# Optimization experiments

Hardware: AMD Instinct MI355X
Metric: run time of the kernel (lower is better)

Reference implementation:

```python
import jax, jax.numpy as jnp
import numpy as np

# --- Instant-NGP hash-grid constants (from __init__ defaults) ---
T = 2 ** 19          # hash table size per level
NLEVELS = 16
F = 2                # features per level
L = 4                # dir positional-encoding frequencies
LEVELS = np.geomspace(16, 2048, NLEVELS, dtype=int)            # grid resolutions
PRIMES = jnp.array([1, 2654435761, 805459861], dtype=jnp.uint32)
FREQS = (2.0 ** np.arange(L)).astype(np.float32)
# corner c in 0..7 -> bit b_i = use ceil along dim i (matches torch corner order)
BITS = jnp.array([[(c >> i) & 1 for i in range(3)] for c in range(8)], dtype=bool)  # (8,3)


def _hash_encode(pos, table):
    """pos: (P,3) level-scaled positions; table: (T,F). Returns (P,F).
    Spatial hash + gather + trilinear interpolation (== grid_sample trick)."""
    fl = jnp.floor(pos)
    ce = jnp.ceil(pos)
    frac = pos - fl                                             # (P,3) in [0,1)
    corners = jnp.where(BITS[None], ce[:, None, :], fl[:, None, :]).astype(jnp.int32)  # (P,8,3)
    # uint32 wrap-around arithmetic matches torch int64 mod 2^19 (T is a power of 2)
    v = corners.astype(jnp.uint32) * PRIMES                     # (P,8,3)
    h = (v[..., 0] ^ v[..., 1] ^ v[..., 2]) & jnp.uint32(T - 1) # (P,8)
    cf = table[h]                                               # (P,8,F) irregular gather
    w = jnp.prod(jnp.where(BITS[None], frac[:, None, :], 1.0 - frac[:, None, :]), axis=-1)  # (P,8)
    return jnp.einsum('pc,pcf->pf', w, cf)


def setup_inputs() -> dict:
    key = jax.random.key(0)
    ks = jax.random.split(key, 16)
    N, S = 2048, 192
    # positions s.t. x*scene_scale + 0.5 lies mostly in (0,1), a few outside (mask path)
    x = (jax.random.uniform(ks[0], (N, S, 3), jnp.float32) - 0.5) * 1.1
    r_dir = jax.random.normal(ks[1], (N, S, 3), jnp.float32)
    tables = jax.random.normal(ks[2], (NLEVELS, T, F), jnp.float32) * 1e-4

    def lin(k, fan_in, fan_out):
        return jax.random.normal(k, (fan_in, fan_out), jnp.float32) / np.float32(np.sqrt(fan_in))

    din = F * NLEVELS              # 32
    cin = 16 + 3 + 3 * L * 2       # 43
    return {
        'x': x, 'r_dir': r_dir, 'tables': tables,
        'dW1': lin(ks[3], din, 64), 'db1': jnp.zeros((64,), jnp.float32),
        'dW2': lin(ks[4], 64, 16), 'db2': jnp.zeros((16,), jnp.float32),
        'cW1': lin(ks[5], cin, 64), 'cb1': jnp.zeros((64,), jnp.float32),
        'cW2': lin(ks[6], 64, 64), 'cb2': jnp.zeros((64,), jnp.float32),
        'cW3': lin(ks[7], 64, 3), 'cb3': jnp.zeros((3,), jnp.float32),
    }


def reference(x, r_dir, tables, dW1, db1, dW2, db2, cW1, cb1, cW2, cb2, cW3, cb3):
    scene_scale = 1.0
    N, S = x.shape[0], r_dir.shape[1]
    xf = x.reshape(-1, 3) * scene_scale + 0.5          # (P,3)
    rd = r_dir.reshape(-1, 3)                          # (P,3)
    mask = jnp.all(xf > 0, axis=-1) & jnp.all(xf < 1, axis=-1)  # (P,)

    # multi-resolution hash encoding (fixed 16-level loop, vectorized over points)
    feats = jnp.concatenate(
        [_hash_encode(xf * np.float32(LEVELS[i]), tables[i]) for i in range(NLEVELS)],
        axis=-1)                                       # (P, F*NLEVELS)

    log_sigma = jax.nn.relu(feats @ dW1 + db1) @ dW2 + db2        # (P,16)

    # direction positional encoding: [dir, sin(2^l*2pi*dir), cos(...)] -> (P, 3+3*2L)
    xin = rd[..., None] * (2.0 * np.pi * jnp.asarray(FREQS))      # (P,3,L)
    enc = jnp.concatenate([jnp.sin(xin), jnp.cos(xin)], axis=-1).reshape(rd.shape[0], -1)
    enc_dir = jnp.concatenate([rd, enc], axis=-1)                 # (P,27)

    h = jax.nn.relu(jnp.concatenate([log_sigma, enc_dir], axis=-1) @ cW1 + cb1)
    h = jax.nn.relu(h @ cW2 + cb2)
    color = jax.nn.sigmoid(h @ cW3 + cb3)                         # (P,3)

    color = jnp.where(mask[:, None], color, 0.0)
    sigma = jnp.where(mask[:, None], jnp.exp(log_sigma[:, :1]), 0.0)
    return color.reshape(N, S, 3), sigma.reshape(N, S, 1)
```

## Files before the change

### kernel.cpp

```cpp
#include <hip/hip_runtime.h>
#include <hip/hip_bf16.h>
#include <cstdint>

#define NPTS (2048 * 192)
#define TBL  (1u << 19)
#define TMASK (TBL - 1u)
#define PBLOCKS (NPTS / 256)
#define ENC_BLOCKS (PBLOCKS * 16)
#define PREP_BLOCKS 6
#define MLP_BLOCKS 1536
#define P2 2654435761u
#define P3 805459861u

__constant__ float LVLS[16] = {16.f, 22.f, 30.f, 42.f, 58.f, 80.f, 111.f, 153.f,
                               212.f, 294.f, 406.f, 561.f, 776.f, 1072.f, 1482.f, 2048.f};

__device__ __forceinline__ uint32_t f2bf(float f) {
    uint32_t u = __float_as_uint(f);
    return (u + 0x7FFFu + ((u >> 16) & 1u)) >> 16;
}
__device__ __forceinline__ uint32_t pack2(float a, float b) {
    return f2bf(a) | (f2bf(b) << 16);
}
__device__ __forceinline__ uint32_t pack2t(float a, float b) {
    return __builtin_amdgcn_perm(__float_as_uint(b), __float_as_uint(a),
                                 0x07060302u);
}

#if __has_builtin(__builtin_amdgcn_sinf)
#define SIN_REV(x) __builtin_amdgcn_sinf(x)
#else
#define SIN_REV(x) __sinf(6.28318530717958647f * (x))
#endif

typedef __attribute__((ext_vector_type(8))) short bf16x8;
typedef __attribute__((ext_vector_type(4))) float f32x4;

#define MFMA_BF16 __builtin_amdgcn_mfma_f32_16x16x32_bf16

__global__ __launch_bounds__(256) void k_encode(const float* __restrict__ x,
                                                const float* __restrict__ tables,
                                                uint32_t* __restrict__ feats,
                                                const float* __restrict__ dW1,
                                                const float* __restrict__ dW2,
                                                const float* __restrict__ cW1,
                                                const float* __restrict__ cb1,
                                                const float* __restrict__ cW2,
                                                const float* __restrict__ cW3,
                                                uint4* __restrict__ wfrags)
{
    if (blockIdx.x >= ENC_BLOCKS) {
        int t = (blockIdx.x - ENC_BLOCKS) * 256 + threadIdx.x;
        if (t >= 24 * 64) return;
        int frag = t >> 6, lane = t & 63;
        const float* W; const float* bfold = nullptr;
        int OUT, Kact, Mact, k0, m0;
        if (frag < 4)       { W = dW1; OUT = 64; Kact = 32; Mact = 64; k0 = 0;               m0 = frag * 16; }
        else if (frag < 6)  { W = dW2; OUT = 16; Kact = 64; Mact = 16; k0 = (frag - 4) * 32; m0 = 0; }
        else if (frag < 14) { int i = frag - 6;  W = cW1; OUT = 64; Kact = 43; Mact = 64;
                              k0 = (i & 1) * 32; m0 = (i >> 1) * 16; bfold = cb1; }
        else if (frag < 22) { int i = frag - 14; W = cW2; OUT = 64; Kact = 64; Mact = 64;
                              k0 = (i & 1) * 32; m0 = (i >> 1) * 16; }
        else                { W = cW3; OUT = 3;  Kact = 64; Mact = 3;  k0 = (frag - 22) * 32; m0 = 0; }
        int m  = m0 + (lane & 15);
        int kq = k0 + ((lane >> 4) << 3);
        uint32_t d[4];
#pragma unroll
        for (int j = 0; j < 4; ++j) {
            float a0 = 0.f, a1 = 0.f;
            int ka = kq + 2 * j, kb = ka + 1;
            if (m < Mact) {
                a0 = (ka < Kact) ? W[(size_t)ka * OUT + m]
                                 : ((bfold && ka == Kact) ? bfold[m] : 0.f);
                a1 = (kb < Kact) ? W[(size_t)kb * OUT + m]
                                 : ((bfold && kb == Kact) ? bfold[m] : 0.f);
            }
            d[j] = f2bf(a0) | (f2bf(a1) << 16);
        }
        wfrags[t] = make_uint4(d[0], d[1], d[2], d[3]);
        return;
    }

    int xs   = blockIdx.x & 7;
    int i    = blockIdx.x >> 3;
    int half = i / PBLOCKS;
    int pb   = i - half * PBLOCKS;
    int lvl  = xs + (half << 3);
    int p    = pb * 256 + threadIdx.x;

    size_t p3 = (size_t)p * 3;
    float x0 = x[p3 + 0] + 0.5f;
    float x1 = x[p3 + 1] + 0.5f;
    float x2 = x[p3 + 2] + 0.5f;
    size_t oidx = (size_t)lvl * NPTS + p;

    bool m = (x0 > 0.f) && (x0 < 1.f) && (x1 > 0.f) && (x1 < 1.f) &&
             (x2 > 0.f) && (x2 < 1.f);
    if (!m) { feats[oidx] = 0u; return; }

    float s  = LVLS[lvl];
    float px = x0 * s, py = x1 * s, pz = x2 * s;
    float flx = floorf(px), fly = floorf(py), flz = floorf(pz);
    float frx = px - flx,   fry = py - fly,   frz = pz - flz;
    int ix = (int)flx, iy = (int)fly, iz = (int)flz;
    uint32_t ux = (uint32_t)ix, uy = (uint32_t)iy, uz = (uint32_t)iz;

    uint32_t base[4];
    base[0] = (uy * P2) ^ (uz * P3);
    base[1] = ((uy + 1u) * P2) ^ (uz * P3);
    base[2] = (uy * P2) ^ ((uz + 1u) * P3);
    base[3] = ((uy + 1u) * P2) ^ ((uz + 1u) * P3);

    const float2* tb = (const float2*)tables + (size_t)lvl * TBL;

    float2 v[8];
    if ((ix & 1) == 0) {
        const float4* tb4 = (const float4*)tb;
#pragma unroll
        for (int cc = 0; cc < 4; ++cc) {
            uint32_t h0 = (base[cc] ^ ux) & TMASK;
            float4 qv = tb4[h0 >> 1];
            bool hi = (h0 & 1u) != 0u;
            float2 e0 = hi ? make_float2(qv.z, qv.w) : make_float2(qv.x, qv.y);
            float2 e1 = hi ? make_float2(qv.x, qv.y) : make_float2(qv.z, qv.w);
            v[(cc << 1)]     = e0;
            v[(cc << 1) | 1] = e1;
        }
    } else {
        uint32_t h[8];
#pragma unroll
        for (int c = 0; c < 8; ++c)
            h[c] = (base[c >> 1] ^ (ux + (uint32_t)(c & 1))) & TMASK;
#pragma unroll
        for (int c = 0; c < 8; ++c) v[c] = tb[h[c]];
    }

    float f0 = 0.f, f1 = 0.f;
#pragma unroll
    for (int c = 0; c < 8; ++c) {
        float w = ((c & 1)        ? frx : 1.f - frx)
                * (((c >> 1) & 1) ? fry : 1.f - fry)
                * (((c >> 2) & 1) ? frz : 1.f - frz);
        f0 += w * v[c].x;
        f1 += w * v[c].y;
    }
    feats[oidx] = pack2(f0, f1);
}

__device__ __forceinline__ bf16x8 trans_frag(uint32_t p01a, uint32_t p23a,
                                             uint32_t p01b, uint32_t p23b, int lane)
{
    int q = lane >> 4, col = lane & 15;
    int srcA = (((q & 1) << 1) << 4) | col;
    int srcB = srcA + 16;
    uint32_t a0 = (uint32_t)__shfl((int)p01a, srcA, 64);
    uint32_t b0 = (uint32_t)__shfl((int)p01b, srcA, 64);
    uint32_t a1 = (uint32_t)__shfl((int)p23a, srcA, 64);
    uint32_t b1 = (uint32_t)__shfl((int)p23b, srcA, 64);
    uint32_t a2 = (uint32_t)__shfl((int)p01a, srcB, 64);
    uint32_t b2 = (uint32_t)__shfl((int)p01b, srcB, 64);
    uint32_t a3 = (uint32_t)__shfl((int)p23a, srcB, 64);
    uint32_t b3 = (uint32_t)__shfl((int)p23b, srcB, 64);
    bool hi = q >= 2;
    union { bf16x8 v; uint32_t d[4]; } u;
    u.d[0] = hi ? b0 : a0;
    u.d[1] = hi ? b1 : a1;
    u.d[2] = hi ? b2 : a2;
    u.d[3] = hi ? b3 : a3;
    return u.v;
}

__device__ __forceinline__ float pe_val(int r, float rx, float ry, float rz)
{
    int t = r - 19;
    int d = t >> 3;
    int s = t & 7;
    float comp = (d == 0) ? rx : ((d == 1) ? ry : rz);
    float a = ldexpf(comp, s & 3) + ((s >= 4) ? 0.25f : 0.0f);
    float v = SIN_REV(a);
    if (r == 16) v = rx;
    if (r == 17) v = ry;
    if (r == 18) v = rz;
    if (r == 43) v = 1.0f;
    if (r > 43)  v = 0.0f;
    return v;
}

__global__ __launch_bounds__(256) void k_mlp(const uint32_t* __restrict__ feats,
                                             const uint4* __restrict__ wfrags,
                                             const float* __restrict__ x,
                                             const float* __restrict__ rdir,
                                             const float* __restrict__ db1,
                                             const float* __restrict__ db2,
                                             const float* __restrict__ cb2,
                                             const float* __restrict__ cb3,
                                             float* __restrict__ out)
{
    int lane = threadIdx.x & 63;
    int q = lane >> 4, col = lane & 15;
    int wgid = blockIdx.x * 4 + (threadIdx.x >> 6);

    union { bf16x8 v; uint4 u; } wf;
    bf16x8 A1[4], A2[2], A3[4][2], A4[4][2], A5[2];
#pragma unroll
    for (int mt = 0; mt < 4; ++mt) { wf.u = wfrags[(0 + mt) * 64 + lane]; A1[mt] = wf.v; }
#pragma unroll
    for (int kt = 0; kt < 2; ++kt) { wf.u = wfrags[(4 + kt) * 64 + lane]; A2[kt] = wf.v; }
#pragma unroll
    for (int mt = 0; mt < 4; ++mt)
#pragma unroll
        for (int kt = 0; kt < 2; ++kt) {
            wf.u = wfrags[(6 + 2 * mt + kt) * 64 + lane];  A3[mt][kt] = wf.v;
            wf.u = wfrags[(14 + 2 * mt + kt) * 64 + lane]; A4[mt][kt] = wf.v;
        }
#pragma unroll
    for (int kt = 0; kt < 2; ++kt) { wf.u = wfrags[(22 + kt) * 64 + lane]; A5[kt] = wf.v; }

    for (int it = 0; it < 4; ++it) {
        int g = (wgid * 4 + it) << 4;
        int pt = g + col;
        size_t pt3 = (size_t)pt * 3;

        union { bf16x8 v; uint32_t d[4]; } Bf;
#pragma unroll
        for (int w = 0; w < 4; ++w)
            Bf.d[w] = feats[(size_t)(q * 4 + w) * NPTS + g + col];

        f32x4 T[4];
#pragma unroll
        for (int mt = 0; mt < 4; ++mt) {
            const float4 bb = *(const float4*)&db1[mt * 16 + q * 4];
            f32x4 c; c[0] = bb.x; c[1] = bb.y; c[2] = bb.z; c[3] = bb.w;
            T[mt] = MFMA_BF16(A1[mt], Bf.v, c, 0, 0, 0);
        }
        uint32_t p01[4], p23[4];
#pragma unroll
        for (int mt = 0; mt < 4; ++mt) {
            p01[mt] = pack2t(fmaxf(T[mt][0], 0.f), fmaxf(T[mt][1], 0.f));
            p23[mt] = pack2t(fmaxf(T[mt][2], 0.f), fmaxf(T[mt][3], 0.f));
        }
        bf16x8 Bh0 = trans_frag(p01[0], p23[0], p01[1], p23[1], lane);
        bf16x8 Bh1 = trans_frag(p01[2], p23[2], p01[3], p23[3], lane);

        f32x4 Dls;
        {
            const float4 bb = *(const float4*)&db2[q * 4];
            f32x4 c; c[0] = bb.x; c[1] = bb.y; c[2] = bb.z; c[3] = bb.w;
            Dls = MFMA_BF16(A2[0], Bh0, c, 0, 0, 0);
            Dls = MFMA_BF16(A2[1], Bh1, Dls, 0, 0, 0);
        }
        uint32_t lp01 = pack2t(Dls[0], Dls[1]);
        uint32_t lp23 = pack2t(Dls[2], Dls[3]);

        float rx = rdir[pt3 + 0], ry = rdir[pt3 + 1], rz = rdir[pt3 + 2];

        union { bf16x8 v; uint32_t d[4]; } Ba0, Ba1;
        Ba0.v = trans_frag(lp01, lp23, lp01, lp23, lane);
        {
            int base = q << 3;
#pragma unroll
            for (int j = 0; j < 4; ++j) {
                uint32_t pk = pack2t(pe_val(base + 2 * j, rx, ry, rz),
                                     pe_val(base + 2 * j + 1, rx, ry, rz));
                if (q >= 2) Ba0.d[j] = pk;
            }
        }
        {
            int base = 32 + (q << 3);
#pragma unroll
            for (int j = 0; j < 4; ++j)
                Ba1.d[j] = pack2t(pe_val(base + 2 * j, rx, ry, rz),
                                  pe_val(base + 2 * j + 1, rx, ry, rz));
        }

        f32x4 C1[4];
#pragma unroll
        for (int mt = 0; mt < 4; ++mt) {
            f32x4 c = {0.f, 0.f, 0.f, 0.f};
            c = MFMA_BF16(A3[mt][0], Ba0.v, c, 0, 0, 0);
            C1[mt] = MFMA_BF16(A3[mt][1], Ba1.v, c, 0, 0, 0);
        }
#pragma unroll
        for (int mt = 0; mt < 4; ++mt) {
            p01[mt] = pack2t(fmaxf(C1[mt][0], 0.f), fmaxf(C1[mt][1], 0.f));
            p23[mt] = pack2t(fmaxf(C1[mt][2], 0.f), fmaxf(C1[mt][3], 0.f));
        }
        bf16x8 Bc0 = trans_frag(p01[0], p23[0], p01[1], p23[1], lane);
        bf16x8 Bc1 = trans_frag(p01[2], p23[2], p01[3], p23[3], lane);

        f32x4 C2[4];
#pragma unroll
        for (int mt = 0; mt < 4; ++mt) {
            const float4 bb = *(const float4*)&cb2[mt * 16 + q * 4];
            f32x4 c; c[0] = bb.x; c[1] = bb.y; c[2] = bb.z; c[3] = bb.w;
            c = MFMA_BF16(A4[mt][0], Bc0, c, 0, 0, 0);
            C2[mt] = MFMA_BF16(A4[mt][1], Bc1, c, 0, 0, 0);
        }
#pragma unroll
        for (int mt = 0; mt < 4; ++mt) {
            p01[mt] = pack2t(fmaxf(C2[mt][0], 0.f), fmaxf(C2[mt][1], 0.f));
            p23[mt] = pack2t(fmaxf(C2[mt][2], 0.f), fmaxf(C2[mt][3], 0.f));
        }
        bf16x8 Bd0 = trans_frag(p01[0], p23[0], p01[1], p23[1], lane);
        bf16x8 Bd1 = trans_frag(p01[2], p23[2], p01[3], p23[3], lane);

        f32x4 c5 = {0.f, 0.f, 0.f, 0.f};
        if (q == 0) { c5[0] = cb3[0]; c5[1] = cb3[1]; c5[2] = cb3[2]; }
        f32x4 Dc = MFMA_BF16(A5[0], Bd0, c5, 0, 0, 0);
        Dc = MFMA_BF16(A5[1], Bd1, Dc, 0, 0, 0);

        if (q == 0) {
            float xfx = x[pt3 + 0] + 0.5f;
            float xfy = x[pt3 + 1] + 0.5f;
            float xfz = x[pt3 + 2] + 0.5f;
            bool m = (xfx > 0.f) && (xfx < 1.f) && (xfy > 0.f) && (xfy < 1.f) &&
                     (xfz > 0.f) && (xfz < 1.f);
            out[pt3 + 0] = m ? 1.f / (1.f + __expf(-Dc[0])) : 0.f;
            out[pt3 + 1] = m ? 1.f / (1.f + __expf(-Dc[1])) : 0.f;
            out[pt3 + 2] = m ? 1.f / (1.f + __expf(-Dc[2])) : 0.f;
            out[(size_t)3 * NPTS + pt] = m ? __expf(Dls[0]) : 0.f;
        }
    }
}

extern "C" void kernel_launch(void* const* d_in, const int* in_sizes, int n_in,
                              void* d_out, int out_size, void* d_ws, size_t ws_size,
                              hipStream_t stream) {
    const float* x      = (const float*)d_in[0];
    const float* rdir   = (const float*)d_in[1];
    const float* tables = (const float*)d_in[2];
    const float* dW1 = (const float*)d_in[3];
    const float* db1 = (const float*)d_in[4];
    const float* dW2 = (const float*)d_in[5];
    const float* db2 = (const float*)d_in[6];
    const float* cW1 = (const float*)d_in[7];
    const float* cb1 = (const float*)d_in[8];
    const float* cW2 = (const float*)d_in[9];
    const float* cb2 = (const float*)d_in[10];
    const float* cW3 = (const float*)d_in[11];
    const float* cb3 = (const float*)d_in[12];
    float* out = (float*)d_out;

    uint4*    wfrags = (uint4*)d_ws;
    uint32_t* feats  = (uint32_t*)((char*)d_ws + 32768);

    k_encode<<<ENC_BLOCKS + PREP_BLOCKS, 256, 0, stream>>>(
        x, tables, feats, dW1, dW2, cW1, cb1, cW2, cW3, wfrags);
    k_mlp<<<MLP_BLOCKS, 256, 0, stream>>>(feats, wfrags, x, rdir,
                                          db1, db2, cb2, cb3, out);
}
```

Baseline: 251.6 us.

## Precompute direction encoding in encode kernel and stage MLP weights in LDS

```diff
diff --git a/kernel.cpp b/kernel.cpp
--- a/kernel.cpp
+++ b/kernel.cpp
@@ -8,7 +8,8 @@
 #define PBLOCKS (NPTS / 256)
 #define ENC_BLOCKS (PBLOCKS * 16)
 #define PREP_BLOCKS 6
-#define MLP_BLOCKS 1536
+#define PE_BLOCKS PBLOCKS
+#define MLP_BLOCKS 3072
 #define P2 2654435761u
 #define P3 805459861u
 
@@ -37,6 +38,22 @@
 typedef __attribute__((ext_vector_type(4))) float f32x4;
 
 #define MFMA_BF16 __builtin_amdgcn_mfma_f32_16x16x32_bf16
+
+__device__ __forceinline__ float pe_val(int r, float rx, float ry, float rz)
+{
+    int t = r - 19;
+    int d = t >> 3;
+    int s = t & 7;
+    float comp = (d == 0) ? rx : ((d == 1) ? ry : rz);
+    float a = ldexpf(comp, s & 3) + ((s >= 4) ? 0.25f : 0.0f);
+    float v = SIN_REV(a);
+    if (r == 16) v = rx;
+    if (r == 17) v = ry;
+    if (r == 18) v = rz;
+    if (r == 43) v = 1.0f;
+    if (r > 43)  v = 0.0f;
+    return v;
+}
 
 __global__ __launch_bounds__(256) void k_encode(const float* __restrict__ x,
                                                 const float* __restrict__ tables,
@@ -47,8 +64,21 @@
                                                 const float* __restrict__ cb1,
                                                 const float* __restrict__ cW2,
                                                 const float* __restrict__ cW3,
-                                                uint4* __restrict__ wfrags)
+                                                uint4* __restrict__ wfrags,
+                                                const float* __restrict__ rdir,
+                                                uint32_t* __restrict__ dirs)
 {
+    if (blockIdx.x >= ENC_BLOCKS + PREP_BLOCKS) {
+        int p = (blockIdx.x - ENC_BLOCKS - PREP_BLOCKS) * 256 + threadIdx.x;
+        size_t p3 = (size_t)p * 3;
+        float rx = rdir[p3 + 0], ry = rdir[p3 + 1], rz = rdir[p3 + 2];
+#pragma unroll
+        for (int i = 0; i < 14; ++i)
+            dirs[(size_t)i * NPTS + p] =
+                pack2t(pe_val(16 + 2 * i, rx, ry, rz),
+                       pe_val(17 + 2 * i, rx, ry, rz));
+        return;
+    }
     if (blockIdx.x >= ENC_BLOCKS) {
         int t = (blockIdx.x - ENC_BLOCKS) * 256 + threadIdx.x;
         if (t >= 24 * 64) return;
@@ -170,54 +200,31 @@
     return u.v;
 }
 
-__device__ __forceinline__ float pe_val(int r, float rx, float ry, float rz)
+__global__ __launch_bounds__(256, 4) void k_mlp(const uint32_t* __restrict__ feats,
+                                                const uint4* __restrict__ wfrags,
+                                                const float* __restrict__ x,
+                                                const uint32_t* __restrict__ dirs,
+                                                const float* __restrict__ db1,
+                                                const float* __restrict__ db2,
+                                                const float* __restrict__ cb2,
+                                                const float* __restrict__ cb3,
+                                                float* __restrict__ out)
 {
-    int t = r - 19;
-    int d = t >> 3;
-    int s = t & 7;
-    float comp = (d == 0) ? rx : ((d == 1) ? ry : rz);
-    float a = ldexpf(comp, s & 3) + ((s >= 4) ? 0.25f : 0.0f);
-    float v = SIN_REV(a);
-    if (r == 16) v = rx;
-    if (r == 17) v = ry;
-    if (r == 18) v = rz;
-    if (r == 43) v = 1.0f;
-    if (r > 43)  v = 0.0f;
-    return v;
-}
-
-__global__ __launch_bounds__(256) void k_mlp(const uint32_t* __restrict__ feats,
-                                             const uint4* __restrict__ wfrags,
-                                             const float* __restrict__ x,
-                                             const float* __restrict__ rdir,
-                                             const float* __restrict__ db1,
-                                             const float* __restrict__ db2,
-                                             const float* __restrict__ cb2,
-                                             const float* __restrict__ cb3,
-                                             float* __restrict__ out)
-{
+    __shared__ uint4 wlds[24 * 64];
+#pragma unroll
+    for (int t = 0; t < 6; ++t)
+        wlds[t * 256 + threadIdx.x] = wfrags[t * 256 + threadIdx.x];
+    __syncthreads();
+
     int lane = threadIdx.x & 63;
     int q = lane >> 4, col = lane & 15;
     int wgid = blockIdx.x * 4 + (threadIdx.x >> 6);
 
-    union { bf16x8 v; uint4 u; } wf;
-    bf16x8 A1[4], A2[2], A3[4][2], A4[4][2], A5[2];
-#pragma unroll
-    for (int mt = 0; mt < 4; ++mt) { wf.u = wfrags[(0 + mt) * 64 + lane]; A1[mt] = wf.v; }
-#pragma unroll
-    for (int kt = 0; kt < 2; ++kt) { wf.u = wfrags[(4 + kt) * 64 + lane]; A2[kt] = wf.v; }
-#pragma unroll
-    for (int mt = 0; mt < 4; ++mt)
-#pragma unroll
-        for (int kt = 0; kt < 2; ++kt) {
-            wf.u = wfrags[(6 + 2 * mt + kt) * 64 + lane];  A3[mt][kt] = wf.v;
-            wf.u = wfrags[(14 + 2 * mt + kt) * 64 + lane]; A4[mt][kt] = wf.v;
-        }
-#pragma unroll
-    for (int kt = 0; kt < 2; ++kt) { wf.u = wfrags[(22 + kt) * 64 + lane]; A5[kt] = wf.v; }
-
-    for (int it = 0; it < 4; ++it) {
-        int g = (wgid * 4 + it) << 4;
+#define LDW(f) ({ union { uint4 u_; bf16x8 v_; } w_; w_.u_ = wlds[(f) * 64 + lane]; w_.v_; })
+
+#pragma unroll
+    for (int it = 0; it < 2; ++it) {
+        int g = (wgid * 2 + it) << 4;
         int pt = g + col;
         size_t pt3 = (size_t)pt * 3;
 
@@ -226,12 +233,22 @@
         for (int w = 0; w < 4; ++w)
             Bf.d[w] = feats[(size_t)(q * 4 + w) * NPTS + g + col];
 
+        uint32_t da[4], dbv[4];
+#pragma unroll
+        for (int j = 0; j < 4; ++j) {
+            int pa = ((q - 2) * 4 + j) & 7;
+            da[j] = dirs[(size_t)pa * NPTS + pt];
+            int pb = 8 + q * 4 + j;
+            pb = (pb > 13) ? 13 : pb;
+            dbv[j] = dirs[(size_t)pb * NPTS + pt];
+        }
+
         f32x4 T[4];
 #pragma unroll
         for (int mt = 0; mt < 4; ++mt) {
             const float4 bb = *(const float4*)&db1[mt * 16 + q * 4];
             f32x4 c; c[0] = bb.x; c[1] = bb.y; c[2] = bb.z; c[3] = bb.w;
-            T[mt] = MFMA_BF16(A1[mt], Bf.v, c, 0, 0, 0);
+            T[mt] = MFMA_BF16(LDW(mt), Bf.v, c, 0, 0, 0);
         }
         uint32_t p01[4], p23[4];
 #pragma unroll
@@ -246,39 +263,27 @@
         {
             const float4 bb = *(const float4*)&db2[q * 4];
             f32x4 c; c[0] = bb.x; c[1] = bb.y; c[2] = bb.z; c[3] = bb.w;
-            Dls = MFMA_BF16(A2[0], Bh0, c, 0, 0, 0);
-            Dls = MFMA_BF16(A2[1], Bh1, Dls, 0, 0, 0);
+            Dls = MFMA_BF16(LDW(4), Bh0, c, 0, 0, 0);
+            Dls = MFMA_BF16(LDW(5), Bh1, Dls, 0, 0, 0);
         }
         uint32_t lp01 = pack2t(Dls[0], Dls[1]);
         uint32_t lp23 = pack2t(Dls[2], Dls[3]);
 
-        float rx = rdir[pt3 + 0], ry = rdir[pt3 + 1], rz = rdir[pt3 + 2];
-
         union { bf16x8 v; uint32_t d[4]; } Ba0, Ba1;
         Ba0.v = trans_frag(lp01, lp23, lp01, lp23, lane);
-        {
-            int base = q << 3;
-#pragma unroll
-            for (int j = 0; j < 4; ++j) {
-                uint32_t pk = pack2t(pe_val(base + 2 * j, rx, ry, rz),
-                                     pe_val(base + 2 * j + 1, rx, ry, rz));
-                if (q >= 2) Ba0.d[j] = pk;
-            }
-        }
-        {
-            int base = 32 + (q << 3);
-#pragma unroll
-            for (int j = 0; j < 4; ++j)
-                Ba1.d[j] = pack2t(pe_val(base + 2 * j, rx, ry, rz),
-                                  pe_val(base + 2 * j + 1, rx, ry, rz));
+#pragma unroll
+        for (int j = 0; j < 4; ++j) {
+            Ba0.d[j] = (q >= 2) ? da[j] : Ba0.d[j];
+            bool vld = (q == 0) | ((q == 1) & (j < 2));
+            Ba1.d[j] = vld ? dbv[j] : 0u;
         }
 
         f32x4 C1[4];
 #pragma unroll
         for (int mt = 0; mt < 4; ++mt) {
             f32x4 c = {0.f, 0.f, 0.f, 0.f};
-            c = MFMA_BF16(A3[mt][0], Ba0.v, c, 0, 0, 0);
-            C1[mt] = MFMA_BF16(A3[mt][1], Ba1.v, c, 0, 0, 0);
+            c = MFMA_BF16(LDW(6 + 2 * mt), Ba0.v, c, 0, 0, 0);
+            C1[mt] = MFMA_BF16(LDW(7 + 2 * mt), Ba1.v, c, 0, 0, 0);
         }
 #pragma unroll
         for (int mt = 0; mt < 4; ++mt) {
@@ -293,8 +298,8 @@
         for (int mt = 0; mt < 4; ++mt) {
             const float4 bb = *(const float4*)&cb2[mt * 16 + q * 4];
             f32x4 c; c[0] = bb.x; c[1] = bb.y; c[2] = bb.z; c[3] = bb.w;
-            c = MFMA_BF16(A4[mt][0], Bc0, c, 0, 0, 0);
-            C2[mt] = MFMA_BF16(A4[mt][1], Bc1, c, 0, 0, 0);
+            c = MFMA_BF16(LDW(14 + 2 * mt), Bc0, c, 0, 0, 0);
+            C2[mt] = MFMA_BF16(LDW(15 + 2 * mt), Bc1, c, 0, 0, 0);
         }
 #pragma unroll
         for (int mt = 0; mt < 4; ++mt) {
@@ -306,8 +311,8 @@
 
         f32x4 c5 = {0.f, 0.f, 0.f, 0.f};
         if (q == 0) { c5[0] = cb3[0]; c5[1] = cb3[1]; c5[2] = cb3[2]; }
-        f32x4 Dc = MFMA_BF16(A5[0], Bd0, c5, 0, 0, 0);
-        Dc = MFMA_BF16(A5[1], Bd1, Dc, 0, 0, 0);
+        f32x4 Dc = MFMA_BF16(LDW(22), Bd0, c5, 0, 0, 0);
+        Dc = MFMA_BF16(LDW(23), Bd1, Dc, 0, 0, 0);
 
         if (q == 0) {
             float xfx = x[pt3 + 0] + 0.5f;
@@ -321,6 +326,7 @@
             out[(size_t)3 * NPTS + pt] = m ? __expf(Dls[0]) : 0.f;
         }
     }
+#undef LDW
 }
 
 extern "C" void kernel_launch(void* const* d_in, const int* in_sizes, int n_in,
@@ -343,9 +349,10 @@
 
     uint4*    wfrags = (uint4*)d_ws;
     uint32_t* feats  = (uint32_t*)((char*)d_ws + 32768);
-
-    k_encode<<<ENC_BLOCKS + PREP_BLOCKS, 256, 0, stream>>>(
-        x, tables, feats, dW1, dW2, cW1, cb1, cW2, cW3, wfrags);
-    k_mlp<<<MLP_BLOCKS, 256, 0, stream>>>(feats, wfrags, x, rdir,
+    uint32_t* dirs   = (uint32_t*)((char*)d_ws + 32768 + (size_t)16 * NPTS * 4);
+
+    k_encode<<<ENC_BLOCKS + PREP_BLOCKS + PE_BLOCKS, 256, 0, stream>>>(
+        x, tables, feats, dW1, dW2, cW1, cb1, cW2, cW3, wfrags, rdir, dirs);
+    k_mlp<<<MLP_BLOCKS, 256, 0, stream>>>(feats, wfrags, x, dirs,
                                           db1, db2, cb2, cb3, out);
 }
```

Measured after the change: 244.0 us. -3.0%, faster.
